# Kernel tuning notes

Hardware: AMD Instinct MI355X
Metric: run time of the kernel (lower is better)

Reference implementation:

```python
import jax, jax.numpy as jnp
import numpy as np

ALPHA = 0.2  # leaky_relu negative slope
EPS = 1e-12  # F.normalize eps
N = 8192
E = 262144
DIN = 512
DOUT = 256


def setup_inputs() -> dict:
    key = jax.random.key(0)
    k1, k2, k3, k4, k5 = jax.random.split(key, 5)
    x = jax.random.normal(k1, (N, DIN), dtype=jnp.float32)
    edge_index = jax.random.randint(k2, (2, E), 0, N, dtype=jnp.int64)
    weight = jax.random.normal(k3, (DIN, DOUT), dtype=jnp.float32) * (1.0 / np.sqrt(DIN))
    a = jax.random.normal(k4, (2 * DOUT, 1), dtype=jnp.float32) * (1.0 / np.sqrt(2 * DOUT))
    bias = jnp.zeros((DOUT,), dtype=jnp.float32)
    return {"x": x, "edge_index": edge_index, "weight": weight, "a": a, "bias": bias}


def reference(x, edge_index, weight, a, bias):
    # h: [N, DOUT]
    h = x @ weight
    dout = weight.shape[1]
    # GAT-style additive scores: e[i,j] = leaky_relu(Wh1[i] + Wh2[j])
    Wh1 = h @ a[:dout, :]   # [N, 1]
    Wh2 = h @ a[dout:, :]   # [N, 1]
    e = jax.nn.leaky_relu(Wh1 + Wh2.T, negative_slope=ALPHA)  # [N, N]
    row, col = edge_index[0], edge_index[1]
    # sparse_e.to_dense(): edge entries hold e values (duplicates summed), rest 0
    sparse_dense = jnp.zeros((x.shape[0], x.shape[0]), dtype=e.dtype).at[row, col].add(e[row, col])
    attention = jax.nn.softmax(sparse_dense, axis=1)  # softmax over full dense row incl. zeros
    # dropout is identity in eval mode
    h_pass = attention @ h  # [N, DOUT]
    out = jax.nn.leaky_relu(h_pass, negative_slope=ALPHA)
    norm = jnp.maximum(jnp.linalg.norm(out, ord=2, axis=1, keepdims=True), EPS)
    out = out / norm
    return out + bias
```

## Files before the change

### kernel.cpp

```cpp
#include <hip/hip_runtime.h>

#define NN 8192
#define NE 262144
#define DIN 512
#define DOUT 256
#define LRELU_ALPHA 0.2f
#define RSLOT 96
#define BM 64
#define BN 64
#define BK 64

using bf16x8 = __attribute__((ext_vector_type(8))) short;
using f32x4 = __attribute__((ext_vector_type(4))) float;

__device__ inline unsigned short bf16rne(float f) {
    unsigned u = __float_as_uint(f);
    return (unsigned short)((u + 0x7FFFu + ((u >> 16) & 1u)) >> 16);
}

__device__ inline void split8(const float4 a, const float4 b, bf16x8& hi, bf16x8& lo) {
    unsigned u0 = __float_as_uint(a.x), u1 = __float_as_uint(a.y);
    unsigned u2 = __float_as_uint(a.z), u3 = __float_as_uint(a.w);
    unsigned u4 = __float_as_uint(b.x), u5 = __float_as_uint(b.y);
    unsigned u6 = __float_as_uint(b.z), u7 = __float_as_uint(b.w);
    union { unsigned u[4]; bf16x8 v; } H_, L_;
    H_.u[0] = (u1 & 0xFFFF0000u) | (u0 >> 16);
    H_.u[1] = (u3 & 0xFFFF0000u) | (u2 >> 16);
    H_.u[2] = (u5 & 0xFFFF0000u) | (u4 >> 16);
    H_.u[3] = (u7 & 0xFFFF0000u) | (u6 >> 16);
    float l0 = a.x - __uint_as_float(u0 & 0xFFFF0000u);
    float l1 = a.y - __uint_as_float(u1 & 0xFFFF0000u);
    float l2 = a.z - __uint_as_float(u2 & 0xFFFF0000u);
    float l3 = a.w - __uint_as_float(u3 & 0xFFFF0000u);
    float l4 = b.x - __uint_as_float(u4 & 0xFFFF0000u);
    float l5 = b.y - __uint_as_float(u5 & 0xFFFF0000u);
    float l6 = b.z - __uint_as_float(u6 & 0xFFFF0000u);
    float l7 = b.w - __uint_as_float(u7 & 0xFFFF0000u);
    L_.u[0] = (__float_as_uint(l1) & 0xFFFF0000u) | (__float_as_uint(l0) >> 16);
    L_.u[1] = (__float_as_uint(l3) & 0xFFFF0000u) | (__float_as_uint(l2) >> 16);
    L_.u[2] = (__float_as_uint(l5) & 0xFFFF0000u) | (__float_as_uint(l4) >> 16);
    L_.u[3] = (__float_as_uint(l7) & 0xFFFF0000u) | (__float_as_uint(l6) >> 16);
    hi = H_.v;
    lo = L_.v;
}

__global__ __launch_bounds__(256) void prep_kernel(const float* __restrict__ W,
                                                   short* __restrict__ Wthi,
                                                   short* __restrict__ Wtlo,
                                                   int* __restrict__ cnt,
                                                   float* __restrict__ Wh1,
                                                   float* __restrict__ Wh2,
                                                   float* __restrict__ Htot) {
    int b = blockIdx.x;
    int t = threadIdx.x;
    if (b < DOUT) {
        int n = b;
        float w0 = W[(size_t)(2 * t) * DOUT + n];
        float w1 = W[(size_t)(2 * t + 1) * DOUT + n];
        unsigned u0 = __float_as_uint(w0), u1 = __float_as_uint(w1);
        unsigned hp = (u1 & 0xFFFF0000u) | (u0 >> 16);
        float l0 = w0 - __uint_as_float(u0 & 0xFFFF0000u);
        float l1 = w1 - __uint_as_float(u1 & 0xFFFF0000u);
        unsigned lp = (__float_as_uint(l1) & 0xFFFF0000u) | (__float_as_uint(l0) >> 16);
        ((unsigned*)Wthi)[n * (DIN / 2) + t] = hp;
        ((unsigned*)Wtlo)[n * (DIN / 2) + t] = lp;
    } else {
        int idx = (b - DOUT) * 256 + t;
        if (idx < NN) cnt[idx] = 0;
        else if (idx < 2 * NN) Wh1[idx - NN] = 0.f;
        else if (idx < 3 * NN) Wh2[idx - 2 * NN] = 0.f;
        else if (idx < 3 * NN + DOUT) Htot[idx - 3 * NN] = 0.f;
    }
}

__device__ inline bf16x8 frag_read(const short* lds, int row, int kslot) {
    return *(const bf16x8*)((const char*)lds + row * 128 + ((kslot ^ (row & 7)) << 4));
}

__global__ __launch_bounds__(256) void gemm_edges_kernel(
    const float* __restrict__ X,
    const short* __restrict__ Wthi, const short* __restrict__ Wtlo,
    const float* __restrict__ av, const int* __restrict__ ei,
    int* __restrict__ cnt, int* __restrict__ csr_col,
    unsigned short* __restrict__ Hb, float* __restrict__ Wh1,
    float* __restrict__ Wh2, float* __restrict__ Htot) {
    if (blockIdx.x >= 512) {
        int e = (blockIdx.x - 512) * 256 + threadIdx.x;
        int r = ei[e];
        int c = ei[NE + e];
        int slot = atomicAdd(&cnt[r], 1);
        if (slot < RSLOT) csr_col[r * RSLOT + slot] = c;
        return;
    }
    __shared__ short Ah[BM * BK], Al[BM * BK], Bh[BN * BK], Bl[BN * BK];
    int b = blockIdx.x;
    int m0 = (b & 127) * BM;
    int n0b = (b >> 7) * BN;
    int t = threadIdx.x;
    int w = t >> 6, lane = t & 63;
    int wm = w >> 1, wn = w & 1;
    int lr = lane & 15;
    int klg = lane >> 4;
    int m0w = wm * 32;
    int n0w = wn * 32;

    int srow0 = t >> 3;
    int scs = t & 7;

    f32x4 acc[2][2] = {};
    float4 px[2][2];
    bf16x8 pbh[2], pbl[2];

#pragma unroll
    for (int j = 0; j < 2; ++j) {
        int row = j * 32 + srow0;
        const float* xs = X + (size_t)(m0 + row) * DIN + scs * 8;
        px[j][0] = *(const float4*)xs;
        px[j][1] = *(const float4*)(xs + 4);
        pbh[j] = *(const bf16x8*)(Wthi + (size_t)(n0b + row) * DIN + scs * 8);
        pbl[j] = *(const bf16x8*)(Wtlo + (size_t)(n0b + row) * DIN + scs * 8);
    }

    for (int k0 = 0; k0 < DIN; k0 += BK) {
#pragma unroll
        for (int j = 0; j < 2; ++j) {
            int row = j * 32 + srow0;
            int so = ((scs ^ (row & 7)) << 4);
            bf16x8 hi, lo;
            split8(px[j][0], px[j][1], hi, lo);
            *(bf16x8*)((char*)Ah + row * 128 + so) = hi;
            *(bf16x8*)((char*)Al + row * 128 + so) = lo;
            *(bf16x8*)((char*)Bh + row * 128 + so) = pbh[j];
            *(bf16x8*)((char*)Bl + row * 128 + so) = pbl[j];
        }
        __syncthreads();

        int kn = k0 + BK;
        if (kn < DIN) {
#pragma unroll
            for (int j = 0; j < 2; ++j) {
                int row = j * 32 + srow0;
                const float* xs = X + (size_t)(m0 + row) * DIN + kn + scs * 8;
                px[j][0] = *(const float4*)xs;
                px[j][1] = *(const float4*)(xs + 4);
                pbh[j] = *(const bf16x8*)(Wthi + (size_t)(n0b + row) * DIN + kn + scs * 8);
                pbl[j] = *(const bf16x8*)(Wtlo + (size_t)(n0b + row) * DIN + kn + scs * 8);
            }
        }

#pragma unroll
        for (int ksub = 0; ksub < 2; ++ksub) {
            int ks = ksub * 4 + klg;
            bf16x8 ah0 = frag_read(Ah, m0w + lr, ks);
            bf16x8 ah1 = frag_read(Ah, m0w + 16 + lr, ks);
            bf16x8 al0 = frag_read(Al, m0w + lr, ks);
            bf16x8 al1 = frag_read(Al, m0w + 16 + lr, ks);
            bf16x8 bh0 = frag_read(Bh, n0w + lr, ks);
            bf16x8 bh1 = frag_read(Bh, n0w + 16 + lr, ks);
            bf16x8 bl0 = frag_read(Bl, n0w + lr, ks);
            bf16x8 bl1 = frag_read(Bl, n0w + 16 + lr, ks);

            acc[0][0] = __builtin_amdgcn_mfma_f32_16x16x32_bf16(ah0, bh0, acc[0][0], 0, 0, 0);
            acc[0][1] = __builtin_amdgcn_mfma_f32_16x16x32_bf16(ah0, bh1, acc[0][1], 0, 0, 0);
            acc[1][0] = __builtin_amdgcn_mfma_f32_16x16x32_bf16(ah1, bh0, acc[1][0], 0, 0, 0);
            acc[1][1] = __builtin_amdgcn_mfma_f32_16x16x32_bf16(ah1, bh1, acc[1][1], 0, 0, 0);
            acc[0][0] = __builtin_amdgcn_mfma_f32_16x16x32_bf16(ah0, bl0, acc[0][0], 0, 0, 0);
            acc[0][1] = __builtin_amdgcn_mfma_f32_16x16x32_bf16(ah0, bl1, acc[0][1], 0, 0, 0);
            acc[1][0] = __builtin_amdgcn_mfma_f32_16x16x32_bf16(ah1, bl0, acc[1][0], 0, 0, 0);
            acc[1][1] = __builtin_amdgcn_mfma_f32_16x16x32_bf16(ah1, bl1, acc[1][1], 0, 0, 0);
            acc[0][0] = __builtin_amdgcn_mfma_f32_16x16x32_bf16(al0, bh0, acc[0][0], 0, 0, 0);
            acc[0][1] = __builtin_amdgcn_mfma_f32_16x16x32_bf16(al0, bh1, acc[0][1], 0, 0, 0);
            acc[1][0] = __builtin_amdgcn_mfma_f32_16x16x32_bf16(al1, bh0, acc[1][0], 0, 0, 0);
            acc[1][1] = __builtin_amdgcn_mfma_f32_16x16x32_bf16(al1, bh1, acc[1][1], 0, 0, 0);
        }
        __syncthreads();
    }

    int orow = (lane >> 4) * 4;
#pragma unroll
    for (int mt = 0; mt < 2; ++mt)
#pragma unroll
        for (int nt = 0; nt < 2; ++nt)
#pragma unroll
            for (int r = 0; r < 4; ++r)
                Hb[(size_t)(m0 + m0w + mt * 16 + orow + r) * DOUT + n0b + n0w + nt * 16 + lr] =
                    bf16rne(acc[mt][nt][r]);

    float a1v0 = av[n0b + n0w + lr];
    float a1v1 = av[n0b + n0w + 16 + lr];
    float a2v0 = av[DOUT + n0b + n0w + lr];
    float a2v1 = av[DOUT + n0b + n0w + 16 + lr];
#pragma unroll
    for (int mt = 0; mt < 2; ++mt)
#pragma unroll
        for (int r = 0; r < 4; ++r) {
            float d1 = acc[mt][0][r] * a1v0 + acc[mt][1][r] * a1v1;
            float d2 = acc[mt][0][r] * a2v0 + acc[mt][1][r] * a2v1;
#pragma unroll
            for (int ofs = 1; ofs < 16; ofs <<= 1) {
                d1 += __shfl_xor(d1, ofs);
                d2 += __shfl_xor(d2, ofs);
            }
            if (lr == 0) {
                int row = m0 + m0w + mt * 16 + orow + r;
                atomicAdd(&Wh1[row], d1);
                atomicAdd(&Wh2[row], d2);
            }
        }

#pragma unroll
    for (int nt = 0; nt < 2; ++nt) {
        float s = 0.f;
#pragma unroll
        for (int mt = 0; mt < 2; ++mt)
#pragma unroll
            for (int r = 0; r < 4; ++r) s += acc[mt][nt][r];
        s += __shfl_xor(s, 16);
        s += __shfl_xor(s, 32);
        if (lane < 16) atomicAdd(&Htot[n0b + n0w + nt * 16 + lane], s);
    }
}

__global__ __launch_bounds__(256) void row_kernel(
    const unsigned short* __restrict__ Hb, const float* __restrict__ Wh1,
    const float* __restrict__ Wh2, const float* __restrict__ Htot,
    const int* __restrict__ cnt, const int* __restrict__ csr_col,
    const float* __restrict__ bias, float* __restrict__ out) {
    __shared__ int scols[4][RSLOT];
    __shared__ float svv[4][RSLOT];
    int tid = threadIdx.x;
    int w = tid >> 6, lane = tid & 63;
    int i = blockIdx.x * 4 + w;
    int n = cnt[i];
    n = n < RSLOT ? n : RSLOT;
    int* colp = scols[w];
    float* vvp = svv[w];
    for (int t = lane; t < n; t += 64) colp[t] = csr_col[i * RSLOT + t];
    __syncthreads();

    const float NEG_INF = -__builtin_inff();
    float wh1 = Wh1[i];
    float localD = 0.f;
    float localm = 0.f;
    for (int t = lane; t < n; t += 64) {
        int c = colp[t];
        int k = 0;
        bool first = true;
        for (int q = 0; q < n; ++q) {
            int cq = colp[q];
            k += (cq == c);
            if (cq == c && q < t) first = false;
        }
        float v;
        if (first) {
            float s = wh1 + Wh2[c];
            s = s > 0.f ? s : LRELU_ALPHA * s;
            v = (float)k * s;
            localD += 1.f;
            localm = fmaxf(localm, v);
        } else {
            v = NEG_INF;
        }
        vvp[t] = v;
    }

    float m = localm, D = localD;
#pragma unroll
    for (int ofs = 32; ofs > 0; ofs >>= 1) {
        m = fmaxf(m, __shfl_xor(m, ofs));
        D += __shfl_xor(D, ofs);
    }

    float em = expf(-m);
    float localZ = 0.f;
    for (int t = lane; t < n; t += 64) {
        float v = vvp[t];
        if (v != NEG_INF) localZ += expf(v - m);
    }
    float Z = localZ;
#pragma unroll
    for (int ofs = 32; ofs > 0; ofs >>= 1) Z += __shfl_xor(Z, ofs);
    Z += ((float)NN - D) * em;
    float invZ = 1.f / Z;

    for (int t = lane; t < n; t += 64) {
        float v = vvp[t];
        vvp[t] = (v != NEG_INF) ? (expf(v - m) - em) * invZ : 0.f;
    }
    __syncthreads();

    float4 a4[8];
#pragma unroll
    for (int j = 0; j < 8; ++j) a4[j] = make_float4(0.f, 0.f, 0.f, 0.f);
    int t = 0;
    for (; t + 8 <= n; t += 8) {
#pragma unroll
        for (int j = 0; j < 8; ++j) {
            float wc = vvp[t + j];
            int cc = colp[t + j];
            const ushort4 hv = *(const ushort4*)(Hb + (size_t)cc * DOUT + lane * 4);
            a4[j].x = fmaf(wc, __uint_as_float((unsigned)hv.x << 16), a4[j].x);
            a4[j].y = fmaf(wc, __uint_as_float((unsigned)hv.y << 16), a4[j].y);
            a4[j].z = fmaf(wc, __uint_as_float((unsigned)hv.z << 16), a4[j].z);
            a4[j].w = fmaf(wc, __uint_as_float((unsigned)hv.w << 16), a4[j].w);
        }
    }
    for (; t < n; ++t) {
        float wc = vvp[t];
        int cc = colp[t];
        const ushort4 hv = *(const ushort4*)(Hb + (size_t)cc * DOUT + lane * 4);
        a4[0].x = fmaf(wc, __uint_as_float((unsigned)hv.x << 16), a4[0].x);
        a4[0].y = fmaf(wc, __uint_as_float((unsigned)hv.y << 16), a4[0].y);
        a4[0].z = fmaf(wc, __uint_as_float((unsigned)hv.z << 16), a4[0].z);
        a4[0].w = fmaf(wc, __uint_as_float((unsigned)hv.w << 16), a4[0].w);
    }
#pragma unroll
    for (int j = 1; j < 8; ++j) {
        a4[0].x += a4[j].x; a4[0].y += a4[j].y; a4[0].z += a4[j].z; a4[0].w += a4[j].w;
    }
    float bc = em * invZ;
    const float4 ht = *(const float4*)(Htot + lane * 4);
    float4 acc = a4[0];
    acc.x = fmaf(bc, ht.x, acc.x);
    acc.y = fmaf(bc, ht.y, acc.y);
    acc.z = fmaf(bc, ht.z, acc.z);
    acc.w = fmaf(bc, ht.w, acc.w);

    float4 val;
    val.x = acc.x > 0.f ? acc.x : LRELU_ALPHA * acc.x;
    val.y = acc.y > 0.f ? acc.y : LRELU_ALPHA * acc.y;
    val.z = acc.z > 0.f ? acc.z : LRELU_ALPHA * acc.z;
    val.w = acc.w > 0.f ? acc.w : LRELU_ALPHA * acc.w;

    float ssq = val.x * val.x + val.y * val.y + val.z * val.z + val.w * val.w;
#pragma unroll
    for (int ofs = 32; ofs > 0; ofs >>= 1) ssq += __shfl_xor(ssq, ofs);
    float inv_nrm = 1.f / fmaxf(sqrtf(ssq), 1e-12f);

    const float4 b4 = *(const float4*)(bias + lane * 4);
    float4 o;
    o.x = fmaf(val.x, inv_nrm, b4.x);
    o.y = fmaf(val.y, inv_nrm, b4.y);
    o.z = fmaf(val.z, inv_nrm, b4.z);
    o.w = fmaf(val.w, inv_nrm, b4.w);
    *(float4*)(out + (size_t)i * DOUT + lane * 4) = o;
}

extern "C" void kernel_launch(void* const* d_in, const int* in_sizes, int n_in,
                              void* d_out, int out_size, void* d_ws, size_t ws_size,
                              hipStream_t stream) {
    const float* x = (const float*)d_in[0];
    const int* ei = (const int*)d_in[1];
    const float* w = (const float*)d_in[2];
    const float* a = (const float*)d_in[3];
    const float* bias = (const float*)d_in[4];
    float* out = (float*)d_out;

    float* Wh1 = (float*)d_ws;
    float* Wh2 = Wh1 + NN;
    float* Htot = Wh2 + NN;
    int* cnt = (int*)(Htot + DOUT);
    int* csr_col = cnt + NN;
    unsigned short* Hb = (unsigned short*)(csr_col + (size_t)NN * RSLOT);
    short* wthi = (short*)(Hb + (size_t)NN * DOUT);
    short* wtlo = wthi + (size_t)DOUT * DIN;

    prep_kernel<<<DOUT + 98, 256, 0, stream>>>(w, wthi, wtlo, cnt, Wh1, Wh2, Htot);
    gemm_edges_kernel<<<512 + NE / 256, 256, 0, stream>>>(
        x, wthi, wtlo, a, ei, cnt, csr_col, Hb, Wh1, Wh2, Htot);
    row_kernel<<<NN / 4, 256, 0, stream>>>(Hb, Wh1, Wh2, Htot, cnt, csr_col, bias, out);
}
```

Measured before the change: 57.84 us.

## Prepack W into MFMA fragment order and double-buffer the A tile in LDS

The prep kernel now writes the bf16 hi/lo split of W already arranged in MFMA B-fragment order, so the GEMM loads B fragments straight from global memory into registers instead of staging them through LDS. The A (X) tile is double-buffered in LDS, which leaves one barrier per k-step instead of two, and the split and LDS store of the next tile overlap the current MFMAs. This cuts LDS traffic and synchronisation, but the B fragments are now global loads issued inside the MFMA loop, and every wave that shares a column block loads them again, relying on cache hits.

```diff
diff --git a/kernel.cpp b/kernel.cpp
--- a/kernel.cpp
+++ b/kernel.cpp
@@ -45,27 +45,31 @@
 }
 
 __global__ __launch_bounds__(256) void prep_kernel(const float* __restrict__ W,
-                                                   short* __restrict__ Wthi,
-                                                   short* __restrict__ Wtlo,
+                                                   short* __restrict__ Wfhi,
+                                                   short* __restrict__ Wflo,
                                                    int* __restrict__ cnt,
                                                    float* __restrict__ Wh1,
                                                    float* __restrict__ Wh2,
                                                    float* __restrict__ Htot) {
     int b = blockIdx.x;
     int t = threadIdx.x;
-    if (b < DOUT) {
-        int n = b;
-        float w0 = W[(size_t)(2 * t) * DOUT + n];
-        float w1 = W[(size_t)(2 * t + 1) * DOUT + n];
+    if (b < 256) {
+        int nb16 = b >> 4, kt = b & 15;
+        int lane = t >> 2;
+        int j = (t & 3) * 2;
+        int col = nb16 * 16 + (lane & 15);
+        int krow = kt * 32 + 8 * (lane >> 4) + j;
+        float w0 = W[(size_t)krow * DOUT + col];
+        float w1 = W[(size_t)(krow + 1) * DOUT + col];
         unsigned u0 = __float_as_uint(w0), u1 = __float_as_uint(w1);
         unsigned hp = (u1 & 0xFFFF0000u) | (u0 >> 16);
         float l0 = w0 - __uint_as_float(u0 & 0xFFFF0000u);
         float l1 = w1 - __uint_as_float(u1 & 0xFFFF0000u);
         unsigned lp = (__float_as_uint(l1) & 0xFFFF0000u) | (__float_as_uint(l0) >> 16);
-        ((unsigned*)Wthi)[n * (DIN / 2) + t] = hp;
-        ((unsigned*)Wtlo)[n * (DIN / 2) + t] = lp;
+        ((unsigned*)Wfhi)[b * 256 + t] = hp;
+        ((unsigned*)Wflo)[b * 256 + t] = lp;
     } else {
-        int idx = (b - DOUT) * 256 + t;
+        int idx = (b - 256) * 256 + t;
         if (idx < NN) cnt[idx] = 0;
         else if (idx < 2 * NN) Wh1[idx - NN] = 0.f;
         else if (idx < 3 * NN) Wh2[idx - 2 * NN] = 0.f;
@@ -79,7 +83,7 @@
 
 __global__ __launch_bounds__(256) void gemm_edges_kernel(
     const float* __restrict__ X,
-    const short* __restrict__ Wthi, const short* __restrict__ Wtlo,
+    const short* __restrict__ Wfhi, const short* __restrict__ Wflo,
     const float* __restrict__ av, const int* __restrict__ ei,
     int* __restrict__ cnt, int* __restrict__ csr_col,
     unsigned short* __restrict__ Hb, float* __restrict__ Wh1,
@@ -92,7 +96,7 @@
         if (slot < RSLOT) csr_col[r * RSLOT + slot] = c;
         return;
     }
-    __shared__ short Ah[BM * BK], Al[BM * BK], Bh[BN * BK], Bl[BN * BK];
+    __shared__ short Ah[2][BM * BK], Al[2][BM * BK];
     int b = blockIdx.x;
     int m0 = (b & 127) * BM;
     int n0b = (b >> 7) * BN;
@@ -107,9 +111,14 @@
     int srow0 = t >> 3;
     int scs = t & 7;
 
+    int nbA = (n0b + n0w) >> 4;
+    const short* bh0p = Wfhi + ((size_t)(nbA * 16) * 64 + lane) * 8;
+    const short* bh1p = Wfhi + ((size_t)((nbA + 1) * 16) * 64 + lane) * 8;
+    const short* bl0p = Wflo + ((size_t)(nbA * 16) * 64 + lane) * 8;
+    const short* bl1p = Wflo + ((size_t)((nbA + 1) * 16) * 64 + lane) * 8;
+
     f32x4 acc[2][2] = {};
     float4 px[2][2];
-    bf16x8 pbh[2], pbl[2];
 
 #pragma unroll
     for (int j = 0; j < 2; ++j) {
@@ -117,48 +126,45 @@
         const float* xs = X + (size_t)(m0 + row) * DIN + scs * 8;
         px[j][0] = *(const float4*)xs;
         px[j][1] = *(const float4*)(xs + 4);
-        pbh[j] = *(const bf16x8*)(Wthi + (size_t)(n0b + row) * DIN + scs * 8);
-        pbl[j] = *(const bf16x8*)(Wtlo + (size_t)(n0b + row) * DIN + scs * 8);
-    }
-
-    for (int k0 = 0; k0 < DIN; k0 += BK) {
-#pragma unroll
-        for (int j = 0; j < 2; ++j) {
-            int row = j * 32 + srow0;
-            int so = ((scs ^ (row & 7)) << 4);
-            bf16x8 hi, lo;
-            split8(px[j][0], px[j][1], hi, lo);
-            *(bf16x8*)((char*)Ah + row * 128 + so) = hi;
-            *(bf16x8*)((char*)Al + row * 128 + so) = lo;
-            *(bf16x8*)((char*)Bh + row * 128 + so) = pbh[j];
-            *(bf16x8*)((char*)Bl + row * 128 + so) = pbl[j];
-        }
+    }
+#pragma unroll
+    for (int j = 0; j < 2; ++j) {
+        int row = j * 32 + srow0;
+        int so = (scs ^ (row & 7)) << 4;
+        bf16x8 hi, lo;
+        split8(px[j][0], px[j][1], hi, lo);
+        *(bf16x8*)((char*)Ah[0] + row * 128 + so) = hi;
+        *(bf16x8*)((char*)Al[0] + row * 128 + so) = lo;
+    }
+
+    for (int i = 0; i < 8; ++i) {
         __syncthreads();
 
-        int kn = k0 + BK;
-        if (kn < DIN) {
+        if (i < 7) {
+            int kn = (i + 1) * BK;
 #pragma unroll
             for (int j = 0; j < 2; ++j) {
                 int row = j * 32 + srow0;
                 const float* xs = X + (size_t)(m0 + row) * DIN + kn + scs * 8;
                 px[j][0] = *(const float4*)xs;
                 px[j][1] = *(const float4*)(xs + 4);
-                pbh[j] = *(const bf16x8*)(Wthi + (size_t)(n0b + row) * DIN + kn + scs * 8);
-                pbl[j] = *(const bf16x8*)(Wtlo + (size_t)(n0b + row) * DIN + kn + scs * 8);
             }
         }
 
+        const short* Ab = Ah[i & 1];
+        const short* Alb = Al[i & 1];
 #pragma unroll
         for (int ksub = 0; ksub < 2; ++ksub) {
             int ks = ksub * 4 + klg;
-            bf16x8 ah0 = frag_read(Ah, m0w + lr, ks);
-            bf16x8 ah1 = frag_read(Ah, m0w + 16 + lr, ks);
-            bf16x8 al0 = frag_read(Al, m0w + lr, ks);
-            bf16x8 al1 = frag_read(Al, m0w + 16 + lr, ks);
-            bf16x8 bh0 = frag_read(Bh, n0w + lr, ks);
-            bf16x8 bh1 = frag_read(Bh, n0w + 16 + lr, ks);
-            bf16x8 bl0 = frag_read(Bl, n0w + lr, ks);
-            bf16x8 bl1 = frag_read(Bl, n0w + 16 + lr, ks);
+            size_t bo = (size_t)(i * 2 + ksub) * 512;
+            bf16x8 bh0 = *(const bf16x8*)(bh0p + bo);
+            bf16x8 bh1 = *(const bf16x8*)(bh1p + bo);
+            bf16x8 bl0 = *(const bf16x8*)(bl0p + bo);
+            bf16x8 bl1 = *(const bf16x8*)(bl1p + bo);
+            bf16x8 ah0 = frag_read(Ab, m0w + lr, ks);
+            bf16x8 ah1 = frag_read(Ab, m0w + 16 + lr, ks);
+            bf16x8 al0 = frag_read(Alb, m0w + lr, ks);
+            bf16x8 al1 = frag_read(Alb, m0w + 16 + lr, ks);
 
             acc[0][0] = __builtin_amdgcn_mfma_f32_16x16x32_bf16(ah0, bh0, acc[0][0], 0, 0, 0);
             acc[0][1] = __builtin_amdgcn_mfma_f32_16x16x32_bf16(ah0, bh1, acc[0][1], 0, 0, 0);
@@ -173,7 +179,18 @@
             acc[1][0] = __builtin_amdgcn_mfma_f32_16x16x32_bf16(al1, bh0, acc[1][0], 0, 0, 0);
             acc[1][1] = __builtin_amdgcn_mfma_f32_16x16x32_bf16(al1, bh1, acc[1][1], 0, 0, 0);
         }
-        __syncthreads();
+
+        if (i < 7) {
+#pragma unroll
+            for (int j = 0; j < 2; ++j) {
+                int row = j * 32 + srow0;
+                int so = (scs ^ (row & 7)) << 4;
+                bf16x8 hi, lo;
+                split8(px[j][0], px[j][1], hi, lo);
+                *(bf16x8*)((char*)Ah[(i + 1) & 1] + row * 128 + so) = hi;
+                *(bf16x8*)((char*)Al[(i + 1) & 1] + row * 128 + so) = lo;
+            }
+        }
     }
 
     int orow = (lane >> 4) * 4;
@@ -362,11 +379,11 @@
     int* cnt = (int*)(Htot + DOUT);
     int* csr_col = cnt + NN;
     unsigned short* Hb = (unsigned short*)(csr_col + (size_t)NN * RSLOT);
-    short* wthi = (short*)(Hb + (size_t)NN * DOUT);
-    short* wtlo = wthi + (size_t)DOUT * DIN;
-
-    prep_kernel<<<DOUT + 98, 256, 0, stream>>>(w, wthi, wtlo, cnt, Wh1, Wh2, Htot);
+    short* wfhi = (short*)(Hb + (size_t)NN * DOUT);
+    short* wflo = wfhi + (size_t)DOUT * DIN;
+
+    prep_kernel<<<256 + 98, 256, 0, stream>>>(w, wfhi, wflo, cnt, Wh1, Wh2, Htot);
     gemm_edges_kernel<<<512 + NE / 256, 256, 0, stream>>>(
-        x, wthi, wtlo, a, ei, cnt, csr_col, Hb, Wh1, Wh2, Htot);
+        x, wfhi, wflo, a, ei, cnt, csr_col, Hb, Wh1, Wh2, Htot);
     row_kernel<<<NN / 4, 256, 0, stream>>>(Hb, Wh1, Wh2, Htot, cnt, csr_col, bias, out);
 }
```

Result: slower. 60.07 us (+3.9%).
